# Optimization experiments

Measured on AMD Instinct MI355X. Metric: run time of the kernel, lower is better.

## Reference

```python
import jax, jax.numpy as jnp
import numpy as np

B, S, IN, H = 8, 8192, 64, 256
HEADS, DH, M, L = 8, 32, 64, 4
FF, NC = 4 * H, 2


def setup_inputs() -> dict:
    key = jax.random.key(0)
    ks = jax.random.split(key, 16)
    w = lambda k, shape, s=0.02: jax.random.normal(k, shape, jnp.float32) * s
    return {
        "x": jax.random.normal(ks[0], (B, S, IN), jnp.float32),
        "emb_w": w(ks[1], (IN, H)), "emb_b": jnp.zeros((H,), jnp.float32),
        "pos": jax.random.normal(ks[2], (1, S, H), jnp.float32),
        "ln1_g": jnp.ones((L, H), jnp.float32), "ln1_b": jnp.zeros((L, H), jnp.float32),
        "wq": w(ks[3], (L, H, H)), "wk": w(ks[4], (L, H, H)), "wv": w(ks[5], (L, H, H)),
        "wo": w(ks[6], (L, H, H)), "bo": jnp.zeros((L, H), jnp.float32),
        "ln2_g": jnp.ones((L, H), jnp.float32), "ln2_b": jnp.zeros((L, H), jnp.float32),
        "w1": w(ks[7], (L, H, FF)), "b1": jnp.zeros((L, FF), jnp.float32),
        "w2": w(ks[8], (L, FF, H)), "b2": jnp.zeros((L, H), jnp.float32),
        "proj": jax.random.normal(ks[9], (L, M, DH), jnp.float32),  # FAVOR+ random features (buffer)
        "fc_w": w(ks[10], (H, NC)), "fc_b": jnp.zeros((NC,), jnp.float32),
    }


def layer_norm(x, g, b, eps=1e-5):
    mu = jnp.mean(x, -1, keepdims=True)
    var = jnp.mean(jnp.square(x - mu), -1, keepdims=True)
    return (x - mu) * jax.lax.rsqrt(var + eps) * g + b


def softmax_kernel(x, proj, is_query, eps=1e-4):
    # performer_pytorch FAVOR+ softmax kernel. x: [b,h,n,d], proj: [m,d]
    normalizer = x.shape[-1] ** -0.25
    ratio = proj.shape[0] ** -0.5
    xp = jnp.einsum('bhnd,md->bhnm', x * normalizer, proj)
    diag = jnp.sum(jnp.square(x), -1, keepdims=True) * (0.5 * normalizer * normalizer)
    if is_query:
        mx = jnp.max(xp, axis=-1, keepdims=True)
    else:
        mx = jnp.max(xp, axis=(-1, -2), keepdims=True)
    return ratio * (jnp.exp(xp - diag - mx) + eps)


def performer_attn(x, wq, wk, wv, wo, bo, proj):
    b, s, h = x.shape
    split = lambda t: t.reshape(b, s, HEADS, DH).transpose(0, 2, 1, 3)
    q, k, v = split(x @ wq), split(x @ wk), split(x @ wv)
    qp = softmax_kernel(q, proj, True)   # [b,h,n,m]
    kp = softmax_kernel(k, proj, False)  # [b,h,n,m]
    d_inv = 1.0 / jnp.einsum('bhnm,bhm->bhn', qp, jnp.sum(kp, axis=2))
    context = jnp.einsum('bhnm,bhne->bhme', kp, v)       # [b,h,m,dh]
    out = jnp.einsum('bhnm,bhme->bhne', qp, context) * d_inv[..., None]
    out = out.transpose(0, 2, 1, 3).reshape(b, s, h)
    return out @ wo + bo


def reference(x, emb_w, emb_b, pos, ln1_g, ln1_b, wq, wk, wv, wo, bo,
              ln2_g, ln2_b, w1, b1, w2, b2, proj, fc_w, fc_b):
    h = x @ emb_w + emb_b + pos[:, :x.shape[1], :]
    for l in range(L):
        h = h + performer_attn(layer_norm(h, ln1_g[l], ln1_b[l]),
                               wq[l], wk[l], wv[l], wo[l], bo[l], proj[l])
        hn = layer_norm(h, ln2_g[l], ln2_b[l])
        h = h + (jax.nn.gelu(hn @ w1[l] + b1[l], approximate=False) @ w2[l] + b2[l])
    pooled = jnp.mean(h, axis=1)
    return pooled @ fc_w + fc_b
```

## Files before the change

### kernel.cpp

```cpp
#include <hip/hip_runtime.h>
#include <math.h>

typedef unsigned short u16;
typedef __attribute__((ext_vector_type(8))) short bf16x8;
typedef __attribute__((ext_vector_type(4))) float f32x4;

static constexpr int D_S = 8192;
static constexpr int D_L = 4;
static constexpr int TOK = 65536;
static constexpr float NORMALIZER = 0.4204482076268573f;
static constexpr float RATIO = 0.125f;
static constexpr float KEPS = 1e-4f;

static constexpr size_t OFF_H     = 0;
static constexpr size_t OFF_XNB   = 16777216;
static constexpr size_t OFF_BIG   = 25165824;
static constexpr size_t OFF_V     = 41943040;
static constexpr size_t OFF_WKP   = 46137344;
static constexpr size_t OFF_WQP   = 46268416;
static constexpr size_t OFF_WK    = 46399488;
static constexpr size_t OFF_WQ    = 46465024;
static constexpr size_t OFF_WV    = 46530560;
static constexpr size_t OFF_WO    = 46596096;
static constexpr size_t OFF_W1    = 46661632;
static constexpr size_t OFF_W2    = 46923776;
static constexpr size_t OFF_DG    = 47185920;
static constexpr size_t OFF_KMAX  = 47710208;
static constexpr size_t OFF_PART  = 47710272;
static constexpr size_t OFF_PARTK = 49807424;
static constexpr size_t OFF_CTX   = 49872960;
static constexpr size_t OFF_KSUM  = 50004032;
static constexpr size_t OFF_POOL  = 50008128;
static constexpr size_t NEED_BYTES = 200040704;

static constexpr int BTS = 136;

static __device__ __forceinline__ float bf2f(u16 u) {
  return __uint_as_float(((unsigned int)u) << 16);
}
static __device__ __forceinline__ u16 f2bf(float f) {
  unsigned int u = __float_as_uint(f);
  u = (u + 0x7fffu + ((u >> 16) & 1u)) >> 16;
  return (u16)u;
}
static __device__ __forceinline__ float geluf(float v) {
  return 0.5f * v * (1.f + erff(v * 0.70710678118654752f));
}
static __device__ __forceinline__ float dec_max(unsigned int mk) {
  return __uint_as_float((mk & 0x80000000u) ? (mk & 0x7fffffffu) : ~mk);
}

static __device__ __forceinline__ void gload16(const u16* g, u16* l) {
  __builtin_amdgcn_global_load_lds(
      (const __attribute__((address_space(1))) unsigned int*)g,
      (__attribute__((address_space(3))) unsigned int*)l, 16, 0, 0);
}

__global__ void report_kernel(float* out, float v) {
  if (threadIdx.x < 16) out[threadIdx.x] = v;
}

__global__ __launch_bounds__(256) void zero_kernel(float* p, int n) {
  int i = blockIdx.x * 256 + threadIdx.x;
  if (i < n) p[i] = 0.f;
}

__global__ __launch_bounds__(256) void xcvt_kernel(const float* __restrict__ x,
                                                   u16* __restrict__ xb) {
  int i4 = (blockIdx.x * 256 + threadIdx.x) * 4;
  float4 v = *(const float4*)(x + i4);
  u16 o[4] = {f2bf(v.x), f2bf(v.y), f2bf(v.z), f2bf(v.w)};
  *(uint2*)(xb + i4) = *(uint2*)o;
}

__global__ __launch_bounds__(256) void ln_kernel(
    const float* __restrict__ src, u16* __restrict__ dst,
    const float* __restrict__ g, const float* __restrict__ b) {
  int wv = threadIdx.x >> 6, lane = threadIdx.x & 63;
  int t = blockIdx.x * 4 + wv;
  const float4 v = *(const float4*)(src + (size_t)t * 256 + lane * 4);
  float s1 = v.x + v.y + v.z + v.w;
  float s2 = v.x * v.x + v.y * v.y + v.z * v.z + v.w * v.w;
  for (int off = 32; off; off >>= 1) {
    s1 += __shfl_xor(s1, off);
    s2 += __shfl_xor(s2, off);
  }
  float mu = s1 * (1.f / 256.f);
  float var = s2 * (1.f / 256.f) - mu * mu;
  float rs = rsqrtf(var + 1e-5f);
  float4 gg = *(const float4*)(g + lane * 4);
  float4 bb = *(const float4*)(b + lane * 4);
  u16 o0 = f2bf((v.x - mu) * rs * gg.x + bb.x);
  u16 o1 = f2bf((v.y - mu) * rs * gg.y + bb.y);
  u16 o2 = f2bf((v.z - mu) * rs * gg.z + bb.z);
  u16 o3 = f2bf((v.w - mu) * rs * gg.w + bb.w);
  uint2 pk;
  pk.x = (unsigned)o0 | ((unsigned)o1 << 16);
  pk.y = (unsigned)o2 | ((unsigned)o3 << 16);
  *(uint2*)(dst + (size_t)t * 256 + lane * 4) = pk;
}

__global__ __launch_bounds__(256) void wsplit_kernel(
    const float* __restrict__ W, u16* __restrict__ Wt, int K, int N, int nb) {
  int i = blockIdx.x * 256 + threadIdx.x;
  int k = i >> nb, n = i & (N - 1);
  float val = W[i];
  u16 hi = f2bf(val);
  u16 lo = f2bf(val - bf2f(hi));
  Wt[(size_t)n * 2 * K + k] = hi;
  Wt[(size_t)n * 2 * K + K + k] = lo;
}

__global__ __launch_bounds__(256) void wprep_kernel(
    const float* __restrict__ wk, const float* __restrict__ wq,
    const float* __restrict__ wv, const float* __restrict__ wo,
    const float* __restrict__ w1, const float* __restrict__ w2,
    const float* __restrict__ proj,
    u16* __restrict__ WKP, u16* __restrict__ WQP,
    u16* __restrict__ WKt, u16* __restrict__ WQt,
    u16* __restrict__ WVt, u16* __restrict__ WOt,
    u16* __restrict__ W1t, u16* __restrict__ W2t,
    unsigned int* __restrict__ kmaxk) {
  int gi = blockIdx.x * 256 + threadIdx.x;
  if (gi < 64) kmaxk[gi] = 0u;
  if (gi < 262144) {
    int i = gi & 131071;
    const float* w = (gi < 131072) ? wk : wq;
    u16* Wt = (gi < 131072) ? WKP : WQP;
    int k = i & 255, n = i >> 8;
    int head = n >> 6, m = n & 63;
    float s = 0.f;
#pragma unroll
    for (int d = 0; d < 32; ++d) s += w[k * 256 + head * 32 + d] * proj[m * 32 + d];
    Wt[(size_t)n * 256 + k] = f2bf(s * NORMALIZER);
  } else if (gi < 393216) {
    int i = gi - 262144;
    const float* W = (i < 65536) ? wk : wq;
    u16* T = (i < 65536) ? WKt : WQt;
    int j = i & 65535;
    int k = j >> 8, n = j & 255;
    T[(size_t)n * 256 + k] = f2bf(W[j]);
  } else if (gi < 524288) {
    int i = gi - 393216;
    const float* W = (i < 65536) ? wv : wo;
    u16* T = (i < 65536) ? WVt : WOt;
    int j = i & 65535;
    int k = j >> 8, n = j & 255;
    T[(size_t)n * 256 + k] = f2bf(W[j]);
  } else if (gi < 786432) {
    int i = gi - 524288;
    int k = i >> 10, n = i & 1023;
    W1t[(size_t)n * 256 + k] = f2bf(w1[i]);
  } else {
    int i = gi - 786432;
    int k = i >> 8, n = i & 255;
    W2t[(size_t)n * 1024 + k] = f2bf(w2[i]);
  }
}

template <int EPI, int ACT, int ACC, int OBF, int KM>
__global__ __launch_bounds__(256) void mfma_gemm(
    const u16* __restrict__ A, const u16* __restrict__ Wt,
    const u16* __restrict__ Wt2,
    const float* __restrict__ bias, const float* __restrict__ posP,
    const u16* __restrict__ diagIn,
    float* __restrict__ outF, u16* __restrict__ outB,
    u16* __restrict__ diagOut, unsigned int* __restrict__ kmaxOut,
    int N, int K) {
  __shared__ __align__(16) u16 Als[12288];
  __shared__ __align__(16) u16 Bls[12288];
  const int K2 = K * KM;
  int tid = threadIdx.x;
  int tot = gridDim.x * gridDim.y;
  int f = blockIdx.x + gridDim.x * blockIdx.y;
  int wid = (f & 7) * (tot >> 3) + (f >> 3);
  int ny = gridDim.y;
  int lg = 31 - __clz(ny);
  int xb = wid >> lg;
  int yb = wid & (ny - 1);
  int bm = xb * 128;
  const u16* Wp = Wt;
  int bn = yb * 128;
  if (EPI == 6 && yb >= 4) { Wp = Wt2; bn = (yb - 4) * 128; }
  int w = tid >> 6, lane = tid & 63;
  int wm = w >> 1, wn = w & 1;
  int lr = lane & 15, lq = lane >> 4;
  f32x4 acc[4][4];
#pragma unroll
  for (int i = 0; i < 4; ++i)
#pragma unroll
    for (int j = 0; j < 4; ++j) acc[i][j] = (f32x4){0.f, 0.f, 0.f, 0.f};
  int sub = lane >> 2;
  int qsw = (lane & 3) ^ ((lane >> 3) & 3);
  const u16* gA0 = A + (size_t)(bm + 32 * w + sub) * K + qsw * 8;
  const u16* gA1 = gA0 + (size_t)16 * K;
  const u16* gB0 = Wp + (size_t)(bn + 32 * w + sub) * K2 + qsw * 8;
  const u16* gB1 = gB0 + (size_t)16 * K2;
  u16* lA0 = Als + (w * 2 + 0) * 512;
  u16* lA1 = Als + (w * 2 + 1) * 512;
  u16* lB0 = Bls + (w * 2 + 0) * 512;
  u16* lB1 = Bls + (w * 2 + 1) * 512;
  int qswr = lq ^ ((lr >> 1) & 3);
  int aB = wm * 256 + lr * 4 + qswr;
  int bB = wn * 256 + lr * 4 + qswr;

#define STAGE(buf, kk) do { \
    int ka_ = (kk) & (K - 1); int kb_ = (kk); int lo_ = (buf) * 4096; \
    gload16(gA0 + ka_, lA0 + lo_); \
    gload16(gA1 + ka_, lA1 + lo_); \
    gload16(gB0 + kb_, lB0 + lo_); \
    gload16(gB1 + kb_, lB1 + lo_); \
  } while (0)

  const int nt = K2 / 32;
  STAGE(0, 0);
  STAGE(1, 32);
  STAGE(2, 64);
  int cur = 0;
  for (int t = 0; t < nt; ++t) {
    if (t + 2 < nt)      asm volatile("s_waitcnt vmcnt(8)" ::: "memory");
    else if (t + 1 < nt) asm volatile("s_waitcnt vmcnt(4)" ::: "memory");
    else                 asm volatile("s_waitcnt vmcnt(0)" ::: "memory");
    __builtin_amdgcn_s_barrier();
    __builtin_amdgcn_sched_barrier(0);
    const bf16x8* Ab = (const bf16x8*)(Als + cur * 4096);
    const bf16x8* Bb = (const bf16x8*)(Bls + cur * 4096);
    bf16x8 af[4], bfr[4];
#pragma unroll
    for (int mi = 0; mi < 4; ++mi) af[mi] = Ab[aB + mi * 64];
#pragma unroll
    for (int ni = 0; ni < 4; ++ni) bfr[ni] = Bb[bB + ni * 64];
#pragma unroll
    for (int mi = 0; mi < 4; ++mi)
#pragma unroll
      for (int ni = 0; ni < 4; ++ni)
        acc[mi][ni] = __builtin_amdgcn_mfma_f32_16x16x32_bf16(af[mi], bfr[ni], acc[mi][ni], 0, 0, 0);
    asm volatile("s_waitcnt lgkmcnt(0)" ::: "memory");
    __builtin_amdgcn_sched_barrier(0);
    __builtin_amdgcn_s_barrier();
    __builtin_amdgcn_sched_barrier(0);
    if (t + 3 < nt) STAGE(cur, (t + 3) * 32);
    cur = (cur == 2) ? 0 : cur + 1;
  }
#undef STAGE
  if (EPI == 0) {
#pragma unroll
    for (int ni = 0; ni < 4; ++ni) {
      int col = bn + wn * 64 + ni * 16 + lr;
      float bv = bias ? bias[col] : 0.f;
#pragma unroll
      for (int mi = 0; mi < 4; ++mi)
#pragma unroll
        for (int rr = 0; rr < 4; ++rr) {
          int rowg = bm + wm * 64 + mi * 16 + lq * 4 + rr;
          float val = acc[mi][ni][rr] + bv;
          if (ACT) val = geluf(val);
          size_t o = (size_t)rowg * N + col;
          if (OBF) outB[o] = f2bf(val);
          else if (ACC) outF[o] += val;
          else outF[o] = val;
        }
    }
  }
  if (EPI == 3) {
    int head = (bn + wn * 64) >> 6;
#pragma unroll
    for (int mi = 0; mi < 4; ++mi) {
      float rm[4] = {-3.4e38f, -3.4e38f, -3.4e38f, -3.4e38f};
#pragma unroll
      for (int ni = 0; ni < 4; ++ni)
#pragma unroll
        for (int rr = 0; rr < 4; ++rr) rm[rr] = fmaxf(rm[rr], acc[mi][ni][rr]);
#pragma unroll
      for (int rr = 0; rr < 4; ++rr) {
        float t = rm[rr];
        t = fmaxf(t, __shfl_xor(t, 1)); t = fmaxf(t, __shfl_xor(t, 2));
        t = fmaxf(t, __shfl_xor(t, 4)); t = fmaxf(t, __shfl_xor(t, 8));
        rm[rr] = t;
      }
#pragma unroll
      for (int rr = 0; rr < 4; ++rr) {
        int rowg = bm + wm * 64 + mi * 16 + lq * 4 + rr;
        float dgv = bf2f(diagIn[(size_t)rowg * 16 + 8 + head]);
#pragma unroll
        for (int ni = 0; ni < 4; ++ni) {
          int col = bn + wn * 64 + ni * 16 + lr;
          float v = RATIO * (__expf(acc[mi][ni][rr] - dgv - rm[rr]) + KEPS);
          outB[(size_t)rowg * N + col] = f2bf(v);
        }
      }
    }
  }
  if (EPI == 4) {
#pragma unroll
    for (int ni = 0; ni < 4; ++ni) {
      int col = bn + wn * 64 + ni * 16 + lr;
      float bv = bias[col];
#pragma unroll
      for (int mi = 0; mi < 4; ++mi)
#pragma unroll
        for (int rr = 0; rr < 4; ++rr) {
          int rowg = bm + wm * 64 + mi * 16 + lq * 4 + rr;
          outF[(size_t)rowg * 256 + col] =
              acc[mi][ni][rr] + bv + posP[(size_t)(rowg & (D_S - 1)) * 256 + col];
        }
    }
  }
  if (EPI == 6) {
    if (yb < 4) {
      float mx = -3.4e38f;
#pragma unroll
      for (int mi = 0; mi < 4; ++mi)
#pragma unroll
        for (int ni = 0; ni < 4; ++ni)
#pragma unroll
          for (int rr = 0; rr < 4; ++rr) {
            float v = acc[mi][ni][rr];
            mx = fmaxf(mx, v);
            int rowg = bm + wm * 64 + mi * 16 + lq * 4 + rr;
            int col = bn + wn * 64 + ni * 16 + lr;
            outB[(size_t)rowg * N + col] = f2bf(v);
          }
#pragma unroll
      for (int off = 1; off < 64; off <<= 1) mx = fmaxf(mx, __shfl_xor(mx, off));
      if (lane == 0) {
        int b = bm >> 13;
        int head = (bn + wn * 64) >> 6;
        unsigned int u = __float_as_uint(mx);
        unsigned int key = (u & 0x80000000u) ? ~u : (u | 0x80000000u);
        atomicMax(kmaxOut + b * 8 + head, key);
      }
    } else {
      const float c05n2 = 0.5f * NORMALIZER * NORMALIZER;
      int hb = (bn + wn * 64) >> 5;
#pragma unroll
      for (int mi = 0; mi < 4; ++mi) {
        float s0[4] = {0.f, 0.f, 0.f, 0.f}, s1[4] = {0.f, 0.f, 0.f, 0.f};
#pragma unroll
        for (int ni = 0; ni < 4; ++ni)
#pragma unroll
          for (int rr = 0; rr < 4; ++rr) {
            float v = acc[mi][ni][rr];
            if (ni < 2) s0[rr] += v * v; else s1[rr] += v * v;
          }
#pragma unroll
        for (int rr = 0; rr < 4; ++rr) {
          float a = s0[rr], b = s1[rr];
          a += __shfl_xor(a, 1); a += __shfl_xor(a, 2); a += __shfl_xor(a, 4); a += __shfl_xor(a, 8);
          b += __shfl_xor(b, 1); b += __shfl_xor(b, 2); b += __shfl_xor(b, 4); b += __shfl_xor(b, 8);
          if (lr == 0) {
            int rowg = bm + wm * 64 + mi * 16 + lq * 4 + rr;
            diagOut[(size_t)rowg * 16 + hb] = f2bf(c05n2 * a);
            diagOut[(size_t)rowg * 16 + hb + 1] = f2bf(c05n2 * b);
          }
        }
      }
    }
  }
}

__global__ __launch_bounds__(256) void ctxaccum_kernel(
    const u16* __restrict__ xp, const u16* __restrict__ v,
    const u16* __restrict__ dg, const unsigned int* __restrict__ kmaxk,
    float* __restrict__ part, float* __restrict__ partk, int hf) {
  __shared__ float kpS[64 * 64];
  __shared__ float vS[64 * 32];
  int tid = threadIdx.x;
  int bl = blockIdx.x >> 3, head = blockIdx.x & 7, c = blockIdx.y;
  int n0l = bl * 8192 + c * 512;
  int bhg = (hf * 4 + bl) * 8 + head;
  int tg0 = hf * 32768 + n0l;
  float mx = dec_max(kmaxk[bhg]);
  int m = tid & 63, eg = tid >> 6;
  float acc[8] = {};
  float ks = 0.f;
  const u16* kpb = xp + (size_t)tg0 * 512 + head * 64;
  const u16* vb = v + (size_t)n0l * 256 + head * 32;
  for (int tile = 0; tile < 8; ++tile) {
    int nb = tile * 64;
    __syncthreads();
#pragma unroll
    for (int i = 0; i < 2; ++i) {
      int idx8 = tid + i * 256;
      int row = idx8 >> 3, c8 = (idx8 & 7) * 8;
      float dgrow = bf2f(dg[(size_t)(tg0 + nb + row) * 16 + head]);
      u16 tmp[8];
      *(uint4*)tmp = *(const uint4*)(kpb + (size_t)(nb + row) * 512 + c8);
#pragma unroll
      for (int j = 0; j < 8; ++j)
        kpS[row * 64 + c8 + j] = RATIO * (__expf(bf2f(tmp[j]) - dgrow - mx) + KEPS);
    }
    {
      int row = tid >> 2, c8 = (tid & 3) * 8;
      u16 tmp[8];
      *(uint4*)tmp = *(const uint4*)(vb + (size_t)(nb + row) * 256 + c8);
#pragma unroll
      for (int j = 0; j < 8; ++j) vS[row * 32 + c8 + j] = bf2f(tmp[j]);
    }
    __syncthreads();
#pragma unroll 4
    for (int n = 0; n < 64; ++n) {
      float kv = kpS[n * 64 + m];
      if (eg == 0) ks += kv;
      const float* vr = &vS[n * 32 + eg * 8];
#pragma unroll
      for (int j = 0; j < 8; ++j) acc[j] += kv * vr[j];
    }
  }
  float* pp = part + ((size_t)bhg * 16 + c) * 2048 + m * 32 + eg * 8;
#pragma unroll
  for (int j = 0; j < 8; ++j) pp[j] = acc[j];
  if (eg == 0) partk[((size_t)bhg * 16 + c) * 64 + m] = ks;
}

__global__ __launch_bounds__(256) void ctxreduce_kernel(
    const float* __restrict__ part, const float* __restrict__ partk,
    float* __restrict__ ctx, float* __restrict__ ksum) {
  int bh = blockIdx.x, tid = threadIdx.x;
#pragma unroll
  for (int i = 0; i < 8; ++i) {
    int idx = tid + i * 256;
    float s = 0.f;
#pragma unroll
    for (int cc = 0; cc < 16; ++cc)
      s += part[((size_t)bh * 16 + cc) * 2048 + idx];
    ctx[(size_t)bh * 2048 + idx] = s;
  }
  if (tid < 64) {
    float s = 0.f;
#pragma unroll
    for (int cc = 0; cc < 16; ++cc) s += partk[((size_t)bh * 16 + cc) * 64 + tid];
    ksum[bh * 64 + tid] = s;
  }
}

__global__ __launch_bounds__(256) void btprep_kernel(
    const float* __restrict__ ctx, const float* __restrict__ ksum,
    u16* __restrict__ Bt) {
  int bh = blockIdx.x, tid = threadIdx.x;
  for (int idx = tid; idx < 48 * 64; idx += 256) {
    int n = idx >> 6, k = idx & 63;
    float v = 0.f;
    if (n < 32) v = ctx[(size_t)bh * 2048 + k * 32 + n];
    else if (n == 32) v = ksum[bh * 64 + k];
    u16 hi = f2bf(v);
    u16 lo = f2bf(v - bf2f(hi));
    u16* row = Bt + ((size_t)bh * 48 + n) * BTS;
    row[k] = hi;
    row[64 + k] = lo;
  }
}

__global__ __launch_bounds__(256) void attnout_kernel(
    const u16* __restrict__ qp, const u16* __restrict__ Bt,
    u16* __restrict__ ao, int hf) {
  __shared__ __align__(16) u16 BtS[48 * BTS];
  int tid = threadIdx.x;
  int rb = blockIdx.x, head = blockIdx.y;
  int t0l = rb * 128;
  int bhg = ((hf * 32768 + t0l) >> 13) * 8 + head;
  {
    const uint4* src = (const uint4*)(Bt + (size_t)bhg * 48 * BTS);
    for (int i = tid; i < 48 * BTS / 8; i += 256) ((uint4*)BtS)[i] = src[i];
  }
  __syncthreads();
  int w = tid >> 6, lane = tid & 63;
  int lr = lane & 15, lq = lane >> 4;
  int tw = t0l + w * 32;
  const u16* qpb = qp + (size_t)(hf * 32768 + tw) * 512 + head * 64;
  bf16x8 af[2][2];
#pragma unroll
  for (int mt = 0; mt < 2; ++mt)
#pragma unroll
    for (int kc = 0; kc < 2; ++kc)
      af[mt][kc] = *(const bf16x8*)(qpb + (size_t)(mt * 16 + lr) * 512 + kc * 32 + lq * 8);
  f32x4 c0[2], c1[2], c2[2];
#pragma unroll
  for (int mt = 0; mt < 2; ++mt) {
    c0[mt] = (f32x4){0.f, 0.f, 0.f, 0.f};
    c1[mt] = (f32x4){0.f, 0.f, 0.f, 0.f};
    c2[mt] = (f32x4){0.f, 0.f, 0.f, 0.f};
  }
#pragma unroll
  for (int kc = 0; kc < 4; ++kc) {
    bf16x8 b0 = *(const bf16x8*)(BtS + (size_t)(0 * 16 + lr) * BTS + kc * 32 + lq * 8);
    bf16x8 b1 = *(const bf16x8*)(BtS + (size_t)(1 * 16 + lr) * BTS + kc * 32 + lq * 8);
    bf16x8 b2 = *(const bf16x8*)(BtS + (size_t)(2 * 16 + lr) * BTS + kc * 32 + lq * 8);
#pragma unroll
    for (int mt = 0; mt < 2; ++mt) {
      bf16x8 a = af[mt][kc & 1];
      c0[mt] = __builtin_amdgcn_mfma_f32_16x16x32_bf16(a, b0, c0[mt], 0, 0, 0);
      c1[mt] = __builtin_amdgcn_mfma_f32_16x16x32_bf16(a, b1, c1[mt], 0, 0, 0);
      c2[mt] = __builtin_amdgcn_mfma_f32_16x16x32_bf16(a, b2, c2[mt], 0, 0, 0);
    }
  }
#pragma unroll
  for (int mt = 0; mt < 2; ++mt)
#pragma unroll
    for (int rr = 0; rr < 4; ++rr) {
      float den = __shfl(c2[mt][rr], lane & 48);
      int rowl = tw + mt * 16 + lq * 4 + rr;
      float inv = 1.f / den;
      ao[(size_t)rowl * 256 + head * 32 + lr] = f2bf(c0[mt][rr] * inv);
      ao[(size_t)rowl * 256 + head * 32 + 16 + lr] = f2bf(c1[mt][rr] * inv);
    }
}

__global__ __launch_bounds__(256) void pool_kernel(
    const float* __restrict__ h, float* __restrict__ pooled) {
  int b = blockIdx.x, chunk = blockIdx.y, j = threadIdx.x;
  const float* hp = h + (size_t)(b * D_S + chunk * 256) * 256 + j;
  float acc = 0.f;
#pragma unroll 4
  for (int s = 0; s < 256; ++s) acc += hp[(size_t)s * 256];
  atomicAdd(pooled + b * 256 + j, acc);
}

__global__ __launch_bounds__(64) void final_kernel(
    const float* __restrict__ pooled, const float* __restrict__ fcw,
    const float* __restrict__ fcb, float* __restrict__ out) {
  int tid = threadIdx.x;
  if (tid >= 16) return;
  int b = tid >> 1, c = tid & 1;
  float acc = 0.f;
  for (int j = 0; j < 256; ++j) acc += pooled[b * 256 + j] * fcw[j * 2 + c];
  out[b * 2 + c] = acc * (1.f / 8192.f) + fcb[c];
}

extern "C" void kernel_launch(void* const* d_in, const int* in_sizes, int n_in,
                              void* d_out, int out_size, void* d_ws, size_t ws_size,
                              hipStream_t stream) {
  const float* x     = (const float*)d_in[0];
  const float* emb_w = (const float*)d_in[1];
  const float* emb_b = (const float*)d_in[2];
  const float* pos   = (const float*)d_in[3];
  const float* ln1_g = (const float*)d_in[4];
  const float* ln1_b = (const float*)d_in[5];
  const float* wq    = (const float*)d_in[6];
  const float* wk    = (const float*)d_in[7];
  const float* wv    = (const float*)d_in[8];
  const float* wo    = (const float*)d_in[9];
  const float* bo    = (const float*)d_in[10];
  const float* ln2_g = (const float*)d_in[11];
  const float* ln2_b = (const float*)d_in[12];
  const float* w1    = (const float*)d_in[13];
  const float* b1    = (const float*)d_in[14];
  const float* w2    = (const float*)d_in[15];
  const float* b2    = (const float*)d_in[16];
  const float* proj  = (const float*)d_in[17];
  const float* fc_w  = (const float*)d_in[18];
  const float* fc_b  = (const float*)d_in[19];

  if (ws_size < NEED_BYTES) {
    report_kernel<<<1, 64, 0, stream>>>((float*)d_out, (float)ws_size);
    return;
  }

  float* ws = (float*)d_ws;
  float* h      = ws + OFF_H;
  u16* xnb      = (u16*)(ws + OFF_XNB);
  u16* BIG      = (u16*)(ws + OFF_BIG);
  u16* Vb       = (u16*)(ws + OFF_V);
  u16* WKPt     = (u16*)(ws + OFF_WKP);
  u16* WQPt     = (u16*)(ws + OFF_WQP);
  u16* WKt      = (u16*)(ws + OFF_WK);
  u16* WQt      = (u16*)(ws + OFF_WQ);
  u16* WVt      = (u16*)(ws + OFF_WV);
  u16* WOt      = (u16*)(ws + OFF_WO);
  u16* W1t      = (u16*)(ws + OFF_W1);
  u16* W2t      = (u16*)(ws + OFF_W2);
  u16* dg       = (u16*)(ws + OFF_DG);
  unsigned int* kmaxk = (unsigned int*)(ws + OFF_KMAX);
  float* part   = ws + OFF_PART;
  u16* Bt       = (u16*)(ws + OFF_PART);
  float* partk  = ws + OFF_PARTK;
  float* ctx    = ws + OFF_CTX;
  float* ksum   = ws + OFF_KSUM;
  float* pooled = ws + OFF_POOL;

  xcvt_kernel<<<4096, 256, 0, stream>>>(x, BIG);
  wsplit_kernel<<<64, 256, 0, stream>>>(emb_w, WKPt, 64, 256, 8);
  mfma_gemm<4, 0, 0, 0, 2><<<dim3(512, 2), 256, 0, stream>>>(
      BIG, WKPt, nullptr, emb_b, pos, nullptr, h, nullptr, nullptr, nullptr, 256, 64);

  for (int l = 0; l < D_L; ++l) {
    const float* pj = proj + l * 2048;
    ln_kernel<<<TOK / 4, 256, 0, stream>>>(h, xnb, ln1_g + l * 256, ln1_b + l * 256);
    wprep_kernel<<<4096, 256, 0, stream>>>(
        wk + l * 65536, wq + l * 65536, wv + l * 65536, wo + l * 65536,
        w1 + l * 262144, w2 + l * 262144, pj,
        WKPt, WQPt, WKt, WQt, WVt, WOt, W1t, W2t, kmaxk);

    mfma_gemm<6, 0, 0, 1, 1><<<dim3(512, 8), 256, 0, stream>>>(
        xnb, WKPt, WKt, nullptr, nullptr, nullptr, nullptr, BIG, dg, kmaxk, 512, 256);
    for (int hf = 0; hf < 2; ++hf) {
      const u16* xh = xnb + (size_t)hf * 32768 * 256;
      mfma_gemm<0, 0, 0, 1, 1><<<dim3(256, 2), 256, 0, stream>>>(
          xh, WVt, nullptr, nullptr, nullptr, nullptr, nullptr, Vb, nullptr, nullptr, 256, 256);
      ctxaccum_kernel<<<dim3(32, 16), 256, 0, stream>>>(BIG, Vb, dg, kmaxk, part, partk, hf);
    }
    ctxreduce_kernel<<<64, 256, 0, stream>>>(part, partk, ctx, ksum);
    btprep_kernel<<<64, 256, 0, stream>>>(ctx, ksum, Bt);
    mfma_gemm<3, 0, 0, 1, 1><<<dim3(512, 4), 256, 0, stream>>>(
        xnb, WQPt, nullptr, nullptr, nullptr, dg, nullptr, BIG, nullptr, nullptr, 512, 256);
    for (int hf = 0; hf < 2; ++hf) {
      float* hh = h + (size_t)hf * 32768 * 256;
      attnout_kernel<<<dim3(256, 8), 256, 0, stream>>>(BIG, Bt, Vb, hf);
      mfma_gemm<0, 0, 1, 0, 1><<<dim3(256, 2), 256, 0, stream>>>(
          Vb, WOt, nullptr, bo + l * 256, nullptr, nullptr, hh, nullptr, nullptr, nullptr, 256, 256);
    }

    ln_kernel<<<TOK / 4, 256, 0, stream>>>(h, xnb, ln2_g + l * 256, ln2_b + l * 256);
    for (int hf = 0; hf < 2; ++hf) {
      const u16* xh = xnb + (size_t)hf * 32768 * 256;
      float* hh = h + (size_t)hf * 32768 * 256;
      mfma_gemm<0, 1, 0, 1, 1><<<dim3(256, 8), 256, 0, stream>>>(
          xh, W1t, nullptr, b1 + l * 1024, nullptr, nullptr, nullptr, BIG, nullptr, nullptr, 1024, 256);
      mfma_gemm<0, 0, 1, 0, 1><<<dim3(256, 2), 256, 0, stream>>>(
          BIG, W2t, nullptr, b2 + l * 256, nullptr, nullptr, hh, nullptr, nullptr, nullptr, 256, 1024);
    }
  }

  zero_kernel<<<8, 256, 0, stream>>>(pooled, 2048);
  pool_kernel<<<dim3(8, 32), 256, 0, stream>>>(h, pooled);
  final_kernel<<<1, 64, 0, stream>>>(pooled, fc_w, fc_b, (float*)d_out);
}
```

Measured before the change: 2.116 ms.

## Process two K-tiles per barrier with four-buffer LDS pipeline and setprio

```diff
diff --git a/kernel.cpp b/kernel.cpp
--- a/kernel.cpp
+++ b/kernel.cpp
@@ -167,8 +167,8 @@
     float* __restrict__ outF, u16* __restrict__ outB,
     u16* __restrict__ diagOut, unsigned int* __restrict__ kmaxOut,
     int N, int K) {
-  __shared__ __align__(16) u16 Als[12288];
-  __shared__ __align__(16) u16 Bls[12288];
+  __shared__ __align__(16) u16 Als[16384];
+  __shared__ __align__(16) u16 Bls[16384];
   const int K2 = K * KM;
   int tid = threadIdx.x;
   int tot = gridDim.x * gridDim.y;
@@ -212,36 +212,46 @@
     gload16(gB1 + kb_, lB1 + lo_); \
   } while (0)
 
-  const int nt = K2 / 32;
+#define FRAGMMA(buf) do { \
+    const bf16x8* Ab_ = (const bf16x8*)(Als + (buf) * 4096); \
+    const bf16x8* Bb_ = (const bf16x8*)(Bls + (buf) * 4096); \
+    bf16x8 af_[4], bfr_[4]; \
+    _Pragma("unroll") \
+    for (int mi = 0; mi < 4; ++mi) af_[mi] = Ab_[aB + mi * 64]; \
+    _Pragma("unroll") \
+    for (int ni = 0; ni < 4; ++ni) bfr_[ni] = Bb_[bB + ni * 64]; \
+    __builtin_amdgcn_s_setprio(1); \
+    _Pragma("unroll") \
+    for (int mi = 0; mi < 4; ++mi) \
+      _Pragma("unroll") \
+      for (int ni = 0; ni < 4; ++ni) \
+        acc[mi][ni] = __builtin_amdgcn_mfma_f32_16x16x32_bf16(af_[mi], bfr_[ni], acc[mi][ni], 0, 0, 0); \
+    __builtin_amdgcn_s_setprio(0); \
+  } while (0)
+
+  const int np = K2 / 64;
   STAGE(0, 0);
   STAGE(1, 32);
   STAGE(2, 64);
-  int cur = 0;
-  for (int t = 0; t < nt; ++t) {
-    if (t + 2 < nt)      asm volatile("s_waitcnt vmcnt(8)" ::: "memory");
-    else if (t + 1 < nt) asm volatile("s_waitcnt vmcnt(4)" ::: "memory");
-    else                 asm volatile("s_waitcnt vmcnt(0)" ::: "memory");
+  STAGE(3, 96);
+  for (int p = 0; p < np; ++p) {
+    int b0 = (p & 1) * 2;
+    if (p + 1 < np) asm volatile("s_waitcnt vmcnt(8)" ::: "memory");
+    else            asm volatile("s_waitcnt vmcnt(0)" ::: "memory");
     __builtin_amdgcn_s_barrier();
     __builtin_amdgcn_sched_barrier(0);
-    const bf16x8* Ab = (const bf16x8*)(Als + cur * 4096);
-    const bf16x8* Bb = (const bf16x8*)(Bls + cur * 4096);
-    bf16x8 af[4], bfr[4];
-#pragma unroll
-    for (int mi = 0; mi < 4; ++mi) af[mi] = Ab[aB + mi * 64];
-#pragma unroll
-    for (int ni = 0; ni < 4; ++ni) bfr[ni] = Bb[bB + ni * 64];
-#pragma unroll
-    for (int mi = 0; mi < 4; ++mi)
-#pragma unroll
-      for (int ni = 0; ni < 4; ++ni)
-        acc[mi][ni] = __builtin_amdgcn_mfma_f32_16x16x32_bf16(af[mi], bfr[ni], acc[mi][ni], 0, 0, 0);
+    FRAGMMA(b0);
+    FRAGMMA(b0 + 1);
     asm volatile("s_waitcnt lgkmcnt(0)" ::: "memory");
     __builtin_amdgcn_sched_barrier(0);
     __builtin_amdgcn_s_barrier();
     __builtin_amdgcn_sched_barrier(0);
-    if (t + 3 < nt) STAGE(cur, (t + 3) * 32);
-    cur = (cur == 2) ? 0 : cur + 1;
-  }
+    if (p + 2 < np) {
+      STAGE(b0, (p + 2) * 64);
+      STAGE(b0 + 1, (p + 2) * 64 + 32);
+    }
+  }
+#undef FRAGMMA
 #undef STAGE
   if (EPI == 0) {
 #pragma unroll
```

After: 2.109 ms. About the same (-0.3%).
